# Kernel tuning notes

Hardware: AMD Instinct MI355X
Metric: run time of the kernel (lower is better)

The kernel has to match this reference:

```python
import jax, jax.numpy as jnp
import numpy as np

N_NODES = 100000


def _gcn_conv(x, W, b, src, dst, num_nodes):
    # x: [N, Fin] -> h: [N, Fout]
    h = x @ W
    # symmetric normalization deg^-1/2[src] * deg^-1/2[dst] (self-loops already appended)
    ones = jnp.ones(src.shape[0], dtype=x.dtype)
    deg = jax.ops.segment_sum(ones, dst, num_segments=num_nodes)
    dinv = jnp.where(deg > 0, jax.lax.rsqrt(deg), 0.0)
    norm = dinv[src] * dinv[dst]  # [E]
    msg = h[src] * norm[:, None]  # [E, Fout] -- dominant memory traffic
    out = jax.ops.segment_sum(msg, dst, num_segments=num_nodes)
    return out + b


def setup_inputs() -> dict:
    key = jax.random.key(0)
    ks = jax.random.split(key, 8)
    N, F_IN, H = N_NODES, 128, 64
    E = 3200000
    x = jax.random.normal(ks[0], (N, F_IN), dtype=jnp.float32)
    edge_index = jax.random.randint(ks[1], (2, E), 0, N, dtype=jnp.int64)
    s1 = 1.0 / np.sqrt(F_IN)
    s2 = 1.0 / np.sqrt(H)
    return {
        "x": x,
        "edge_index": edge_index,
        "W1": jax.random.normal(ks[2], (F_IN, H), dtype=jnp.float32) * s1,
        "b1": jnp.zeros((H,), dtype=jnp.float32),
        "W2": jax.random.normal(ks[3], (H, H), dtype=jnp.float32) * s2,
        "b2": jnp.zeros((H,), dtype=jnp.float32),
        "W_time": jax.random.normal(ks[4], (H, 1), dtype=jnp.float32) * s2,
        "b_time": jnp.zeros((1,), dtype=jnp.float32),
        "W_event": jax.random.normal(ks[5], (H, 1), dtype=jnp.float32) * s2,
        "b_event": jnp.zeros((1,), dtype=jnp.float32),
    }


def reference(x, edge_index, W1, b1, W2, b2, W_time, b_time, W_event, b_event):
    N = x.shape[0]
    # GCNConv default: add self-loops before normalization/aggregation
    loops = jnp.arange(N, dtype=edge_index.dtype)
    src = jnp.concatenate([edge_index[0], loops])
    dst = jnp.concatenate([edge_index[1], loops])

    h = jax.nn.relu(_gcn_conv(x, W1, b1, src, dst, N))
    # dropout is identity in eval mode
    h = jax.nn.relu(_gcn_conv(h, W2, b2, src, dst, N))

    survival_time = h @ W_time + b_time    # [N, 1]
    event_status = h @ W_event + b_event   # [N, 1]
    return survival_time, event_status
```

## Files before the change

### kernel.cpp

```cpp
#include <hip/hip_runtime.h>
#include <math.h>

constexpr int H = 64;
constexpr int FIN = 128;
constexpr int BIN_SHIFT = 7;
constexpr int BIN_NODES = 1 << BIN_SHIFT;
constexpr int MAX_BINS = 1024;
constexpr int BIN_CAP = 5120;
constexpr int SRC_BITS = 25;
constexpr unsigned SRC_MASK = (1u << SRC_BITS) - 1;

typedef __attribute__((ext_vector_type(8))) __bf16 bf16x8;
typedef __attribute__((ext_vector_type(4))) float f32x4;

__device__ inline float bf2f(unsigned short u) {
    unsigned v = ((unsigned)u) << 16;
    return __builtin_bit_cast(float, v);
}
__device__ inline unsigned short f2bf(float f) {
    unsigned u = __builtin_bit_cast(unsigned, f);
    unsigned rnd = 0x7FFFu + ((u >> 16) & 1u);
    return (unsigned short)((u + rnd) >> 16);
}

__device__ inline int wave_incl_scan(int v, int lane) {
#pragma unroll
    for (int off = 1; off < 64; off <<= 1) {
        int t = __shfl_up(v, off);
        if (lane >= off) v += t;
    }
    return v;
}

__global__ void k_initcur(int* __restrict__ cursor, int nbins) {
    int i = blockIdx.x * blockDim.x + threadIdx.x;
    if (i < nbins) cursor[i] = i * BIN_CAP;
}

__global__ __launch_bounds__(256) void k_bin(
    const int* __restrict__ src, const int* __restrict__ dst, int E, int nbins,
    int* __restrict__ cursor, int* __restrict__ binned) {
    __shared__ int hist[MAX_BINS];
    __shared__ int base[MAX_BINS];
    int tid = threadIdx.x;
    long long e0 = (long long)E * blockIdx.x / gridDim.x;
    long long e1 = (long long)E * (blockIdx.x + 1) / gridDim.x;
    for (int i = tid; i < nbins; i += 256) hist[i] = 0;
    __syncthreads();
    for (long long e = e0 + tid; e < e1; e += 256)
        atomicAdd(&hist[dst[e] >> BIN_SHIFT], 1);
    __syncthreads();
    for (int i = tid; i < nbins; i += 256) {
        int h = hist[i];
        base[i] = h ? atomicAdd(&cursor[i], h) : 0;
        hist[i] = 0;
    }
    __syncthreads();
    for (long long e = e0 + tid; e < e1; e += 256) {
        int d = dst[e];
        int b = d >> BIN_SHIFT;
        int r = atomicAdd(&hist[b], 1);
        binned[base[b] + r] = (int)(((unsigned)(d & (BIN_NODES - 1)) << SRC_BITS) | (unsigned)src[e]);
    }
}

__global__ __launch_bounds__(256) void k_binscan(
    const int* __restrict__ cursor, int nbins,
    int* __restrict__ binbase, int* __restrict__ rowptr, int N, int E) {
    __shared__ int wsum[4];
    int tid = threadIdx.x, lane = tid & 63, wid = tid >> 6;
    int b0 = tid * 4;
    int c[4];
#pragma unroll
    for (int k = 0; k < 4; ++k) {
        int b = b0 + k;
        c[k] = (b < nbins) ? cursor[b] - b * BIN_CAP : 0;
    }
    int t = c[0] + c[1] + c[2] + c[3];
    int incl = wave_incl_scan(t, lane);
    if (lane == 63) wsum[wid] = incl;
    __syncthreads();
    int woff = 0;
    for (int w = 0; w < wid; ++w) woff += wsum[w];
    int p = woff + incl - t;
#pragma unroll
    for (int k = 0; k < 4; ++k) {
        int b = b0 + k;
        if (b < nbins) binbase[b] = p;
        p += c[k];
    }
    if (tid == 0) rowptr[N] = E;
}

__global__ __launch_bounds__(256) void k_binsort(
    const int* __restrict__ cursor, const int* __restrict__ binbase,
    const int* __restrict__ binned, int N,
    int* __restrict__ csr_src, int* __restrict__ rowptr, float* __restrict__ dinv) {
    __shared__ int cnt[BIN_NODES];
    __shared__ int excl[BIN_NODES];
    __shared__ int rnk[BIN_NODES];
    __shared__ int wsum[2];
    int bin = blockIdx.x;
    int tid = threadIdx.x, lane = tid & 63, wid = tid >> 6;
    int n = cursor[bin] - bin * BIN_CAP;
    int gbase = binbase[bin];
    const int* bp = binned + (size_t)bin * BIN_CAP;
    if (tid < BIN_NODES) { cnt[tid] = 0; rnk[tid] = 0; }
    __syncthreads();
    for (int i = tid; i < n; i += 256)
        atomicAdd(&cnt[((unsigned)bp[i]) >> SRC_BITS], 1);
    __syncthreads();
    int v = (tid < BIN_NODES) ? cnt[tid] : 0;
    int incl = wave_incl_scan(v, lane);
    if (tid < BIN_NODES && lane == 63) wsum[wid] = incl;
    __syncthreads();
    if (tid < BIN_NODES) {
        int off = (wid == 1) ? wsum[0] : 0;
        int ex = off + incl - v;
        excl[tid] = ex;
        int node = bin * BIN_NODES + tid;
        if (node < N) {
            rowptr[node] = gbase + ex;
            dinv[node] = 1.0f / sqrtf((float)v + 1.0f);
        }
    }
    __syncthreads();
    for (int i = tid; i < n; i += 256) {
        unsigned w = (unsigned)bp[i];
        int dl = w >> SRC_BITS;
        int r = atomicAdd(&rnk[dl], 1);
        csr_src[gbase + excl[dl] + r] = (int)(w & SRC_MASK);
    }
}

template<int K, bool RELU_IN>
__global__ __launch_bounds__(256) void k_mgemm(
    const float* __restrict__ X, const float* __restrict__ W,
    const float* __restrict__ bias, const float* __restrict__ dinv,
    int N, unsigned short* __restrict__ A16) {
    constexpr int LDK = K + 8;
    __shared__ short sX[64 * LDK];
    __shared__ short sWt[64 * LDK];
    int tid = threadIdx.x;
    for (int idx = tid; idx < K * 64; idx += 256) {
        int k = idx >> 6, c = idx & 63;
        sWt[c * LDK + k] = (short)f2bf(W[idx]);
    }
    {
        int row = tid >> 2;
        int q0 = (tid & 3) * (K / 4);
        int grow = blockIdx.x * 64 + row;
        const float* xp = X + (size_t)grow * K + q0;
        unsigned* dstp = (unsigned*)&sX[row * LDK + q0];
#pragma unroll
        for (int i = 0; i < K / 16; ++i) {
            float4 v = make_float4(0.f, 0.f, 0.f, 0.f);
            if (grow < N) v = *(const float4*)(xp + i * 4);
            if (RELU_IN) {
                float4 bb = *(const float4*)(bias + q0 + i * 4);
                v.x = fmaxf(v.x + bb.x, 0.f); v.y = fmaxf(v.y + bb.y, 0.f);
                v.z = fmaxf(v.z + bb.z, 0.f); v.w = fmaxf(v.w + bb.w, 0.f);
            }
            unsigned lo = (unsigned)f2bf(v.x) | ((unsigned)f2bf(v.y) << 16);
            unsigned hi = (unsigned)f2bf(v.z) | ((unsigned)f2bf(v.w) << 16);
            dstp[i * 2] = lo;
            dstp[i * 2 + 1] = hi;
        }
    }
    __syncthreads();
    int w = tid >> 6, lane = tid & 63;
    int mrow = lane & 15, kgrp = lane >> 4;
    f32x4 acc[4] = {};
    const short* xbase = &sX[(16 * w + mrow) * LDK + kgrp * 8];
    const short* wbase = &sWt[mrow * LDK + kgrp * 8];
#pragma unroll
    for (int t = 0; t < K / 32; ++t) {
        bf16x8 a = *(const bf16x8*)(xbase + 32 * t);
#pragma unroll
        for (int c = 0; c < 4; ++c) {
            bf16x8 b = *(const bf16x8*)(wbase + 16 * c * LDK + 32 * t);
            acc[c] = __builtin_amdgcn_mfma_f32_16x16x32_bf16(a, b, acc[c], 0, 0, 0);
        }
    }
    int r0g = blockIdx.x * 64 + 16 * w + kgrp * 4;
#pragma unroll
    for (int r = 0; r < 4; ++r) {
        int rg = r0g + r;
        if (rg < N) {
            float dv = dinv[rg];
#pragma unroll
            for (int c = 0; c < 4; ++c)
                A16[(size_t)rg * H + 16 * c + mrow] = f2bf(acc[c][r] * dv);
        }
    }
}

__device__ inline void addbf4(float4& a, ushort4 u) {
    a.x += bf2f(u.x); a.y += bf2f(u.y); a.z += bf2f(u.z); a.w += bf2f(u.w);
}
__device__ inline void add4(float4& a, const float4& b) {
    a.x += b.x; a.y += b.y; a.z += b.z; a.w += b.w;
}

template<bool FUSE>
__global__ __launch_bounds__(256) void k_gather(
    const int* __restrict__ rowptr, const int* __restrict__ csr_src,
    const float* __restrict__ dinv, const unsigned short* __restrict__ A16,
    float* __restrict__ B, int N,
    const float* __restrict__ b2, const float* __restrict__ Wt, const float* __restrict__ bt,
    const float* __restrict__ We, const float* __restrict__ be, float* __restrict__ out) {
    int node = blockIdx.x * 4 + (threadIdx.x >> 6);
    if (node >= N) return;
    int lane = threadIdx.x & 63;
    int grp = lane >> 4, sub = lane & 15;
    const ushort4* A4 = (const ushort4*)A16;
    int beg = rowptr[node], end = rowptr[node + 1];
    float4 a0 = make_float4(0.f, 0.f, 0.f, 0.f), a1 = a0, a2 = a0, a3 = a0;
    if (grp == 0) addbf4(a0, A4[(size_t)node * 16 + sub]);
    for (int e0 = beg; e0 < end; e0 += 64) {
        int m = end - e0; if (m > 64) m = 64;
        int id = (lane < m) ? csr_src[e0 + lane] : 0;
        int c = 0;
        for (; c + 16 <= m; c += 16) {
            int s0 = __shfl(id, c + grp);
            int s1 = __shfl(id, c + 4 + grp);
            int s2 = __shfl(id, c + 8 + grp);
            int s3 = __shfl(id, c + 12 + grp);
            ushort4 v0 = A4[(size_t)s0 * 16 + sub];
            ushort4 v1 = A4[(size_t)s1 * 16 + sub];
            ushort4 v2 = A4[(size_t)s2 * 16 + sub];
            ushort4 v3 = A4[(size_t)s3 * 16 + sub];
            addbf4(a0, v0); addbf4(a1, v1); addbf4(a2, v2); addbf4(a3, v3);
        }
        for (; c < m; c += 4) {
            int cc = c + grp;
            int s = __shfl(id, cc < m ? cc : 0);
            if (cc < m) addbf4(a0, A4[(size_t)s * 16 + sub]);
        }
    }
    add4(a0, a1); add4(a2, a3); add4(a0, a2);
    a0.x += __shfl_xor(a0.x, 16); a0.y += __shfl_xor(a0.y, 16);
    a0.z += __shfl_xor(a0.z, 16); a0.w += __shfl_xor(a0.w, 16);
    a0.x += __shfl_xor(a0.x, 32); a0.y += __shfl_xor(a0.y, 32);
    a0.z += __shfl_xor(a0.z, 32); a0.w += __shfl_xor(a0.w, 32);
    if (grp == 0) {
        float dv = dinv[node];
        a0.x *= dv; a0.y *= dv; a0.z *= dv; a0.w *= dv;
        if (!FUSE) {
            ((float4*)B)[(size_t)node * 16 + sub] = a0;
        } else {
            int f = sub * 4;
            float g0 = fmaxf(a0.x + b2[f + 0], 0.f);
            float g1 = fmaxf(a0.y + b2[f + 1], 0.f);
            float g2 = fmaxf(a0.z + b2[f + 2], 0.f);
            float g3 = fmaxf(a0.w + b2[f + 3], 0.f);
            float p1 = g0 * Wt[f] + g1 * Wt[f + 1] + g2 * Wt[f + 2] + g3 * Wt[f + 3];
            float p2 = g0 * We[f] + g1 * We[f + 1] + g2 * We[f + 2] + g3 * We[f + 3];
#pragma unroll
            for (int off = 1; off < 16; off <<= 1) {
                p1 += __shfl_xor(p1, off);
                p2 += __shfl_xor(p2, off);
            }
            if (sub == 0) {
                out[node] = p1 + bt[0];
                out[N + node] = p2 + be[0];
            }
        }
    }
}

extern "C" void kernel_launch(void* const* d_in, const int* in_sizes, int n_in,
                              void* d_out, int out_size, void* d_ws, size_t ws_size,
                              hipStream_t stream) {
    const float* x  = (const float*)d_in[0];
    const int* edge = (const int*)d_in[1];
    const float* W1 = (const float*)d_in[2];
    const float* b1 = (const float*)d_in[3];
    const float* W2 = (const float*)d_in[4];
    const float* b2 = (const float*)d_in[5];
    const float* Wt = (const float*)d_in[6];
    const float* bt = (const float*)d_in[7];
    const float* We = (const float*)d_in[8];
    const float* be = (const float*)d_in[9];

    int N = in_sizes[0] / FIN;
    int E = in_sizes[1] / 2;
    const int* src = edge;
    const int* dst = edge + E;
    int nbins = (N + BIN_NODES - 1) >> BIN_SHIFT;

    char* ws = (char*)d_ws;
    size_t off = 0;
    auto alloc = [&](size_t bytes) {
        void* p = ws + off;
        off += (bytes + 255) & ~size_t(255);
        return p;
    };
    float* dinv    = (float*)alloc((size_t)N * sizeof(float));
    int*   rowptr  = (int*)alloc((size_t)(N + 1) * sizeof(int));
    int*   cursor  = (int*)alloc((size_t)nbins * sizeof(int));
    int*   binbase = (int*)alloc((size_t)nbins * sizeof(int));
    int*   binned  = (int*)alloc((size_t)nbins * BIN_CAP * sizeof(int));
    int*   csr_src = (int*)alloc((size_t)E * sizeof(int));
    unsigned short* A16 = (unsigned short*)alloc((size_t)N * H * sizeof(unsigned short));
    float* B       = (float*)alloc((size_t)N * H * sizeof(float));

    k_initcur<<<(nbins + 255) / 256, 256, 0, stream>>>(cursor, nbins);
    k_bin<<<512, 256, 0, stream>>>(src, dst, E, nbins, cursor, binned);
    k_binscan<<<1, 256, 0, stream>>>(cursor, nbins, binbase, rowptr, N, E);
    k_binsort<<<nbins, 256, 0, stream>>>(cursor, binbase, binned, N, csr_src, rowptr, dinv);

    int ggrid = (N + 63) / 64;
    k_mgemm<FIN, false><<<ggrid, 256, 0, stream>>>(x, W1, nullptr, dinv, N, A16);
    k_gather<false><<<(N + 3) / 4, 256, 0, stream>>>(rowptr, csr_src, dinv, A16, B, N,
                                                     nullptr, nullptr, nullptr, nullptr, nullptr, nullptr);

    k_mgemm<H, true><<<ggrid, 256, 0, stream>>>(B, W2, b1, dinv, N, A16);
    k_gather<true><<<(N + 3) / 4, 256, 0, stream>>>(rowptr, csr_src, dinv, A16, nullptr, N,
                                                    b2, Wt, bt, We, be, (float*)d_out);
}
```

Measured before the change: 234.5 us.

## Cache dst reads and bin ranks in registers, widen bins to 256 nodes

The binning kernel now reads dst once, computes each edge's bin and its rank within the block-local histogram in one pass, and keeps the packed result in registers. The scatter pass then reuses it instead of reloading dst and repeating the shared atomics. Edges beyond the unrolled register capacity take a fallback path that uses global atomics. Bins grow to 256 nodes, which halves the bin count and lets every thread of the sort kernel own one node. The risks are higher register pressure and fewer, larger sort blocks, which means less parallelism in k_binsort.

```diff
diff --git a/kernel.cpp b/kernel.cpp
--- a/kernel.cpp
+++ b/kernel.cpp
@@ -3,12 +3,14 @@
 
 constexpr int H = 64;
 constexpr int FIN = 128;
-constexpr int BIN_SHIFT = 7;
+constexpr int BIN_SHIFT = 8;
 constexpr int BIN_NODES = 1 << BIN_SHIFT;
-constexpr int MAX_BINS = 1024;
-constexpr int BIN_CAP = 5120;
-constexpr int SRC_BITS = 25;
+constexpr int MAX_BINS = 512;
+constexpr int BIN_CAP = 10240;
+constexpr int SRC_BITS = 24;
 constexpr unsigned SRC_MASK = (1u << SRC_BITS) - 1;
+constexpr int KB_BLOCKS = 512;
+constexpr int KB_ITER = 25;
 
 typedef __attribute__((ext_vector_type(8))) __bf16 bf16x8;
 typedef __attribute__((ext_vector_type(4))) float f32x4;
@@ -45,22 +47,43 @@
     int tid = threadIdx.x;
     long long e0 = (long long)E * blockIdx.x / gridDim.x;
     long long e1 = (long long)E * (blockIdx.x + 1) / gridDim.x;
+    int chunk = (int)(e1 - e0);
     for (int i = tid; i < nbins; i += 256) hist[i] = 0;
     __syncthreads();
-    for (long long e = e0 + tid; e < e1; e += 256)
-        atomicAdd(&hist[dst[e] >> BIN_SHIFT], 1);
+    int packed[KB_ITER];
+#pragma unroll
+    for (int i = 0; i < KB_ITER; ++i) {
+        int o = i * 256 + tid;
+        packed[i] = -1;
+        if (o < chunk) {
+            int d = dst[e0 + o];
+            int b = d >> BIN_SHIFT;
+            int r = atomicAdd(&hist[b], 1);
+            packed[i] = (b << 22) | ((d & (BIN_NODES - 1)) << 14) | r;
+        }
+    }
     __syncthreads();
     for (int i = tid; i < nbins; i += 256) {
         int h = hist[i];
         base[i] = h ? atomicAdd(&cursor[i], h) : 0;
-        hist[i] = 0;
-    }
-    __syncthreads();
-    for (long long e = e0 + tid; e < e1; e += 256) {
-        int d = dst[e];
+    }
+    __syncthreads();
+#pragma unroll
+    for (int i = 0; i < KB_ITER; ++i) {
+        int o = i * 256 + tid;
+        if (o < chunk) {
+            unsigned w = (unsigned)packed[i];
+            int b = (int)(w >> 22);
+            int dl = (int)((w >> 14) & 0xFF);
+            int r = (int)(w & 0x3FFF);
+            binned[base[b] + r] = (int)(((unsigned)dl << SRC_BITS) | (unsigned)src[e0 + o]);
+        }
+    }
+    for (int o = KB_ITER * 256 + tid; o < chunk; o += 256) {
+        int d = dst[e0 + o];
         int b = d >> BIN_SHIFT;
-        int r = atomicAdd(&hist[b], 1);
-        binned[base[b] + r] = (int)(((unsigned)(d & (BIN_NODES - 1)) << SRC_BITS) | (unsigned)src[e]);
+        int r = atomicAdd(&cursor[b], 1);
+        binned[r] = (int)(((unsigned)(d & (BIN_NODES - 1)) << SRC_BITS) | (unsigned)src[e0 + o]);
     }
 }
 
@@ -99,30 +122,29 @@
     __shared__ int cnt[BIN_NODES];
     __shared__ int excl[BIN_NODES];
     __shared__ int rnk[BIN_NODES];
-    __shared__ int wsum[2];
+    __shared__ int wsum[4];
     int bin = blockIdx.x;
     int tid = threadIdx.x, lane = tid & 63, wid = tid >> 6;
     int n = cursor[bin] - bin * BIN_CAP;
     int gbase = binbase[bin];
     const int* bp = binned + (size_t)bin * BIN_CAP;
-    if (tid < BIN_NODES) { cnt[tid] = 0; rnk[tid] = 0; }
+    cnt[tid] = 0; rnk[tid] = 0;
     __syncthreads();
     for (int i = tid; i < n; i += 256)
         atomicAdd(&cnt[((unsigned)bp[i]) >> SRC_BITS], 1);
     __syncthreads();
-    int v = (tid < BIN_NODES) ? cnt[tid] : 0;
+    int v = cnt[tid];
     int incl = wave_incl_scan(v, lane);
-    if (tid < BIN_NODES && lane == 63) wsum[wid] = incl;
-    __syncthreads();
-    if (tid < BIN_NODES) {
-        int off = (wid == 1) ? wsum[0] : 0;
-        int ex = off + incl - v;
-        excl[tid] = ex;
-        int node = bin * BIN_NODES + tid;
-        if (node < N) {
-            rowptr[node] = gbase + ex;
-            dinv[node] = 1.0f / sqrtf((float)v + 1.0f);
-        }
+    if (lane == 63) wsum[wid] = incl;
+    __syncthreads();
+    int woff = 0;
+    for (int w = 0; w < wid; ++w) woff += wsum[w];
+    int ex = woff + incl - v;
+    excl[tid] = ex;
+    int node = bin * BIN_NODES + tid;
+    if (node < N) {
+        rowptr[node] = gbase + ex;
+        dinv[node] = 1.0f / sqrtf((float)v + 1.0f);
     }
     __syncthreads();
     for (int i = tid; i < n; i += 256) {
@@ -306,7 +328,7 @@
     float* B       = (float*)alloc((size_t)N * H * sizeof(float));
 
     k_initcur<<<(nbins + 255) / 256, 256, 0, stream>>>(cursor, nbins);
-    k_bin<<<512, 256, 0, stream>>>(src, dst, E, nbins, cursor, binned);
+    k_bin<<<KB_BLOCKS, 256, 0, stream>>>(src, dst, E, nbins, cursor, binned);
     k_binscan<<<1, 256, 0, stream>>>(cursor, nbins, binbase, rowptr, N, E);
     k_binsort<<<nbins, 256, 0, stream>>>(cursor, binbase, binned, N, csr_src, rowptr, dinv);
 
```

New measurement: 226.3 us. -3.5%, faster.
